# Performance work log

Measured on AMD Instinct MI355X. Metric: run time of the kernel, lower is better.

The kernel has to match this reference:

```python
import jax, jax.numpy as jnp
import numpy as np

B, N, P = 16, 128, 4096          # images, proposals/img, pairs/img
D_IN, D_HID = 1024, 512          # input_dim, hidden_dim
D_GEO, D_EMB = 128, 200          # geometry_feat_dim, embed_dim
N_OBJ, N_REL = 151, 51           # obj classes, rel classes (out_dim = 50)
OUT = N_REL - 1
LN_EPS = 1e-5


def _ln(x, g, b):
    mu = jnp.mean(x, axis=-1, keepdims=True)
    var = jnp.var(x, axis=-1, keepdims=True)
    return (x - mu) * jax.lax.rsqrt(var + LN_EPS) * g + b


def setup_inputs() -> dict:
    key = jax.random.key(0)
    ks = jax.random.split(key, 20)
    w = lambda k, shape: (jax.random.normal(k, shape, jnp.float32) * 0.02)
    return {
        'visual_feat': jax.random.normal(ks[0], (B * P, D_IN), jnp.float32),
        'box_info': jax.random.uniform(ks[1], (B, N, 9), jnp.float32),
        'pred_logits': jax.random.normal(ks[2], (B, N, N_OBJ), jnp.float32),
        'pair_idx': jax.random.randint(ks[3], (B, P, 2), 0, N, jnp.int32),
        'obj_sem_w': w(ks[4], (N_OBJ, D_EMB)),
        'pos_w1': w(ks[5], (9, D_GEO)), 'pos_b1': jnp.zeros((D_GEO,), jnp.float32),
        'pos_w2': w(ks[6], (D_GEO, D_GEO)), 'pos_b2': jnp.zeros((D_GEO,), jnp.float32),
        'vis_w': w(ks[7], (D_IN, D_HID)), 'vis_b': jnp.zeros((D_HID,), jnp.float32),
        'geo_w': w(ks[8], (2 * D_EMB + 2 * D_GEO, D_HID)), 'geo_b': jnp.zeros((D_HID,), jnp.float32),
        'fus_g': jnp.ones((2 * D_HID,), jnp.float32), 'fus_bt': jnp.zeros((2 * D_HID,), jnp.float32),
        'fus_w': w(ks[9], (2 * D_HID, D_HID)), 'fus_b': jnp.zeros((D_HID,), jnp.float32),
        'cls_g': jnp.ones((D_HID,), jnp.float32), 'cls_bt': jnp.zeros((D_HID,), jnp.float32),
        'cls_w': w(ks[10], (D_HID, OUT)), 'cls_b': jnp.zeros((OUT,), jnp.float32),
    }


def reference(visual_feat, box_info, pred_logits, pair_idx,
              obj_sem_w, pos_w1, pos_b1, pos_w2, pos_b2,
              vis_w, vis_b, geo_w, geo_b,
              fus_g, fus_bt, fus_w, fus_b,
              cls_g, cls_bt, cls_w, cls_b):
    # detach() in torch -> stop_gradient
    vf = jax.lax.stop_gradient(visual_feat)
    pl = jax.lax.stop_gradient(pred_logits)
    # vis_embed = Sequential(ReLU, Linear): [B*P, D_IN] -> [B, P, D_HID]
    vis = (jnp.maximum(vf, 0.0) @ vis_w + vis_b).reshape(B, P, D_HID)
    # obj_pos_embed = Linear, ReLU, Linear: [B, N, 9] -> [B, N, D_GEO]
    pos = jnp.maximum(box_info @ pos_w1 + pos_b1, 0.0) @ pos_w2 + pos_b2
    # semantic embed: softmax over obj classes @ embedding table -> [B, N, D_EMB]
    sem = jax.nn.softmax(pl, axis=-1) @ obj_sem_w
    bidx = jnp.arange(B)[:, None]
    s, o = pair_idx[..., 0], pair_idx[..., 1]
    # gather pair reps: [B, P, 2*(D_GEO+D_EMB)]
    rep = jnp.concatenate([pos[bidx, s], sem[bidx, s], pos[bidx, o], sem[bidx, o]], axis=-1)
    # proposal_box_feat_extract = Sequential(ReLU, Linear)
    geo = jnp.maximum(rep, 0.0) @ geo_w + geo_b
    # proposal_feat_fusion = Sequential(LayerNorm, ReLU, Linear)
    fused = jnp.concatenate([vis, geo], axis=-1)
    fused = jnp.maximum(_ln(fused, fus_g, fus_bt), 0.0) @ fus_w + fus_b
    # proposal_relness_cls_fc = Sequential(LayerNorm, ReLU, Linear)
    logits = jnp.maximum(_ln(fused, cls_g, cls_bt), 0.0) @ cls_w + cls_b  # [B, P, OUT]
    # predictor_type == 'single': scatter max sigmoid score into NxN matrix
    scores = jnp.max(jax.nn.sigmoid(logits), axis=-1)  # [B, P]
    rel_mat = jnp.zeros((B, N, N), logits.dtype).at[bidx, s, o].set(scores)
    return logits.reshape(B * P, OUT), rel_mat
```

## Files before the change

### kernel.cpp

```cpp
#include <hip/hip_runtime.h>
#include <cstdint>

#define B_    16
#define N_    128
#define P_    4096
#define M_    65536
#define DIN   1024
#define DHID  512
#define DGEO  128
#define DEMB  200
#define NODEF 328
#define NOBJ  151
#define OUTC  50
#define KGEO  656
#define KGEOP 672

typedef __attribute__((ext_vector_type(8))) short bf16x8;
typedef __attribute__((ext_vector_type(4))) float f32x4;

typedef __attribute__((address_space(3))) unsigned char lds_u8;
typedef __attribute__((address_space(1))) unsigned char glb_u8;

static __device__ __forceinline__ void async_copy16(const void* g, void* l) {
  __builtin_amdgcn_global_load_lds((const glb_u8*)g, (lds_u8*)l, 16, 0, 0);
}

static __device__ __forceinline__ unsigned short f2b(float f) {
  union { float f; unsigned u; } v; v.f = f;
  unsigned r = v.u + 0x7fffu + ((v.u >> 16) & 1u);
  return (unsigned short)(r >> 16);
}
static __device__ __forceinline__ float b2f(unsigned short b) {
  union { unsigned u; float f; } v; v.u = ((unsigned)b) << 16;
  return v.f;
}
static __device__ __forceinline__ unsigned pack2(float a, float b) {
  return (unsigned)f2b(a) | ((unsigned)f2b(b) << 16);
}
static __device__ __forceinline__ void unpack8(uint4 raw, float* x) {
  x[0] = b2f(raw.x & 0xffffu); x[1] = b2f(raw.x >> 16);
  x[2] = b2f(raw.y & 0xffffu); x[3] = b2f(raw.y >> 16);
  x[4] = b2f(raw.z & 0xffffu); x[5] = b2f(raw.z >> 16);
  x[6] = b2f(raw.w & 0xffffu); x[7] = b2f(raw.w >> 16);
}

#define ZN   131072
#define TV   (512 * 1024)
#define TG   (512 * KGEOP)
#define TF   (512 * 1024)
#define TC   (128 * 512)
#define PREP_TOT (ZN + TV + TG + TF + TC)
__global__ __launch_bounds__(256)
void prep_kernel(uint4* __restrict__ scat,
                 const float* __restrict__ vis_w, unsigned short* __restrict__ wT_vis,
                 const float* __restrict__ geo_w, unsigned short* __restrict__ wT_geo,
                 const float* __restrict__ fus_w, unsigned short* __restrict__ wT_fus,
                 const float* __restrict__ cls_w, unsigned short* __restrict__ wT_cls) {
  int idx = blockIdx.x * 256 + threadIdx.x;
  if (idx < ZN) { scat[idx] = make_uint4(0, 0, 0, 0); return; }
  idx -= ZN;
  if (idx < TV) {
    int n = idx >> 10, k = idx & 1023;
    wT_vis[idx] = f2b(vis_w[(size_t)k * 512 + n]);
    return;
  }
  idx -= TV;
  if (idx < TG) {
    int n = idx / KGEOP, k = idx - n * KGEOP;
    wT_geo[idx] = (k < KGEO) ? f2b(geo_w[(size_t)k * 512 + n]) : 0;
    return;
  }
  idx -= TG;
  if (idx < TF) {
    int n = idx >> 10, k = idx & 1023;
    wT_fus[idx] = f2b(fus_w[(size_t)k * 512 + n]);
    return;
  }
  idx -= TF;
  if (idx < TC) {
    int n = idx >> 9, k = idx & 511;
    wT_cls[idx] = (n < OUTC) ? f2b(cls_w[(size_t)k * OUTC + n]) : 0;
  }
}

__global__ __launch_bounds__(128)
void node_kernel(const float* __restrict__ box, const float* __restrict__ plog,
                 const float* __restrict__ semw,
                 const float* __restrict__ w1, const float* __restrict__ b1,
                 const float* __restrict__ w2, const float* __restrict__ b2,
                 unsigned short* __restrict__ nodeFb) {
  const int node = blockIdx.x;
  const int t = threadIdx.x;
  __shared__ float sBox[9];
  __shared__ float sH[128];
  __shared__ float sE[NOBJ];
  __shared__ float sRed[4];
  if (t < 9) sBox[t] = box[node * 9 + t];
  float l0 = (t < NOBJ) ? plog[node * NOBJ + t] : -1e30f;
  float l1 = (t + 128 < NOBJ) ? plog[node * NOBJ + t + 128] : -1e30f;
  __syncthreads();
  float h = b1[t];
#pragma unroll
  for (int i = 0; i < 9; i++) h = fmaf(sBox[i], w1[i * 128 + t], h);
  h = fmaxf(h, 0.f);
  sH[t] = h;
  float mx = fmaxf(l0, l1);
#pragma unroll
  for (int off = 32; off >= 1; off >>= 1) mx = fmaxf(mx, __shfl_xor(mx, off));
  if ((t & 63) == 0) sRed[t >> 6] = mx;
  __syncthreads();
  mx = fmaxf(sRed[0], sRed[1]);
  float e0 = (t < NOBJ) ? expf(l0 - mx) : 0.f;
  float e1 = (t + 128 < NOBJ) ? expf(l1 - mx) : 0.f;
  if (t < NOBJ) sE[t] = e0;
  if (t + 128 < NOBJ) sE[t + 128] = e1;
  float sm = e0 + e1;
#pragma unroll
  for (int off = 32; off >= 1; off >>= 1) sm += __shfl_xor(sm, off);
  if ((t & 63) == 0) sRed[2 + (t >> 6)] = sm;
  __syncthreads();
  const float inv = 1.f / (sRed[2] + sRed[3]);
  float pv = b2[t];
  for (int i = 0; i < 128; i++) pv = fmaf(sH[i], w2[i * 128 + t], pv);
  nodeFb[(size_t)node * NODEF + t] = f2b(fmaxf(pv, 0.f));
  float a0 = 0.f, a1 = 0.f;
  const int d1 = (t + 128 < DEMB) ? (t + 128) : 0;
  for (int i = 0; i < NOBJ; i++) {
    float e = sE[i];
    a0 = fmaf(e, semw[i * DEMB + t], a0);
    a1 = fmaf(e, semw[i * DEMB + d1], a1);
  }
  nodeFb[(size_t)node * NODEF + 128 + t] = f2b(fmaxf(a0 * inv, 0.f));
  if (t + 128 < DEMB) nodeFb[(size_t)node * NODEF + 128 + t + 128] = f2b(fmaxf(a1 * inv, 0.f));
}

__global__ __launch_bounds__(256)
void stats_kernel(const unsigned short* __restrict__ X, float* __restrict__ st) {
  const int lane = threadIdx.x & 63, wv = threadIdx.x >> 6;
  const size_t row = (size_t)blockIdx.x * 4 + wv;
  const unsigned short* xp = X + row * 1024 + lane * 16;
  float x[16];
  uint4 r0 = *(const uint4*)(xp);
  uint4 r1 = *(const uint4*)(xp + 8);
  unpack8(r0, x); unpack8(r1, x + 8);
  float s = 0.f, s2 = 0.f;
#pragma unroll
  for (int q = 0; q < 16; q++) { s += x[q]; s2 = fmaf(x[q], x[q], s2); }
#pragma unroll
  for (int off = 32; off >= 1; off >>= 1) { s += __shfl_xor(s, off); s2 += __shfl_xor(s2, off); }
  if (lane == 0) {
    float mu = s * (1.f / 1024.f);
    float var = s2 * (1.f / 1024.f) - mu * mu;
    ((float2*)st)[row] = make_float2(mu, rsqrtf(var + 1e-5f));
  }
}

template<int D>
__global__ __launch_bounds__(256)
void ln_relu_kernel(unsigned short* __restrict__ X,
                    const float* __restrict__ g, const float* __restrict__ bta) {
  constexpr int C = D / 64;
  const int lane = threadIdx.x & 63, wv = threadIdx.x >> 6;
  const size_t row = (size_t)blockIdx.x * 4 + wv;
  unsigned short* xp = X + row * D + lane * C;
  float x[C];
#pragma unroll
  for (int c = 0; c < C; c += 8) {
    uint4 raw = *(const uint4*)(xp + c);
    unpack8(raw, x + c);
  }
  float s = 0.f, s2 = 0.f;
#pragma unroll
  for (int q = 0; q < C; q++) { s += x[q]; s2 = fmaf(x[q], x[q], s2); }
#pragma unroll
  for (int off = 32; off >= 1; off >>= 1) { s += __shfl_xor(s, off); s2 += __shfl_xor(s2, off); }
  const float mu = s / D;
  const float rs = rsqrtf(s2 / D - mu * mu + 1e-5f);
  const float* gp = g + lane * C;
  const float* bp = bta + lane * C;
#pragma unroll
  for (int c = 0; c < C; c += 8) {
    float4 g0 = *(const float4*)(gp + c), g1 = *(const float4*)(gp + c + 4);
    float4 t0 = *(const float4*)(bp + c), t1 = *(const float4*)(bp + c + 4);
    float y0 = fmaxf(fmaf((x[c + 0] - mu) * rs, g0.x, t0.x), 0.f);
    float y1 = fmaxf(fmaf((x[c + 1] - mu) * rs, g0.y, t0.y), 0.f);
    float y2 = fmaxf(fmaf((x[c + 2] - mu) * rs, g0.z, t0.z), 0.f);
    float y3 = fmaxf(fmaf((x[c + 3] - mu) * rs, g0.w, t0.w), 0.f);
    float y4 = fmaxf(fmaf((x[c + 4] - mu) * rs, g1.x, t1.x), 0.f);
    float y5 = fmaxf(fmaf((x[c + 5] - mu) * rs, g1.y, t1.y), 0.f);
    float y6 = fmaxf(fmaf((x[c + 6] - mu) * rs, g1.z, t1.z), 0.f);
    float y7 = fmaxf(fmaf((x[c + 7] - mu) * rs, g1.w, t1.w), 0.f);
    uint4 u;
    u.x = pack2(y0, y1); u.y = pack2(y2, y3);
    u.z = pack2(y4, y5); u.w = pack2(y6, y7);
    *(uint4*)(xp + c) = u;
  }
}

static __device__ __forceinline__ int pair_swz(int bid, int nwg) {
  const int cpx2 = nwg >> 4;
  const int pr = bid >> 1, q = bid & 1;
  return (((pr & 7) * cpx2) + (pr >> 3)) * 2 + q;
}

template<int MODE>
__global__ __launch_bounds__(512, 4)
void gemm128x256g(const unsigned short* __restrict__ A, int ldaE,
                  const unsigned short* __restrict__ Bt, int Ktot,
                  const float* __restrict__ bias,
                  unsigned short* __restrict__ C, int ldcE, int ccol0,
                  int NS, int NBN,
                  const int* __restrict__ pidx,
                  const unsigned short* __restrict__ nodeFb,
                  const unsigned short* __restrict__ zsrc) {
  __shared__ __align__(16) unsigned char smem[49152];
  const int tid = threadIdx.x;
  const int lane = tid & 63, w = tid >> 6;
  const int swz = pair_swz(blockIdx.x, gridDim.x);
  const int bm = swz / NBN, bn = swz - bm * NBN;

  const int sslot = (tid & 3) ^ ((tid >> 3) & 3);
  const int srow = tid >> 2;
  const size_t ldaBy = (size_t)ldaE * 2, ldbBy = (size_t)Ktot * 2;
  const unsigned char* aG = (const unsigned char*)A + (size_t)(bm * 128 + srow) * ldaBy + sslot * 16;
  const unsigned char* bG = (const unsigned char*)Bt + (size_t)(bn * 256 + srow) * ldbBy + sslot * 16;

  const unsigned short* nbS = nullptr;
  const unsigned short* nbO = nullptr;
  if (MODE == 2) {
    int pr = bm * 128 + srow;
    int2 so = *(const int2*)(pidx + 2 * pr);
    int b = pr >> 12;
    nbS = nodeFb + (size_t)((b << 7) + so.x) * NODEF;
    nbO = nodeFb + (size_t)((b << 7) + so.y) * NODEF;
  }

  auto stage = [&](int s) {
    const int slot = s & 1;
    unsigned char* la = smem + slot * 8192 + w * 1024;
    unsigned char* lb = smem + 16384 + slot * 16384 + w * 1024;
    if (MODE == 0) {
      async_copy16(aG + (size_t)s * 64, la);
    } else {
      const int e = s * 32 + sslot * 8;
      uintptr_t sel = (e < NODEF) ? (uintptr_t)(nbS + e)
                    : (e < KGEO)  ? (uintptr_t)(nbO + (e - NODEF))
                                  : (uintptr_t)zsrc;
      async_copy16((const void*)sel, la);
    }
    const unsigned char* sb = bG + (size_t)s * 64;
    async_copy16(sb, lb);
    async_copy16(sb + 128 * ldbBy, lb + 8192);
  };

  const int wm = w >> 2, wn = w & 3;
  const int frow = lane & 15;
  const int colb = (((lane >> 4) ^ ((frow >> 1) & 3)) << 4);
  const int aRowB = (wm * 64 + frow) * 64;
  const int bRowB = (wn * 64 + frow) * 64;

  f32x4 acc[4][4];
#pragma unroll
  for (int m = 0; m < 4; m++)
#pragma unroll
    for (int n = 0; n < 4; n++) acc[m][n] = (f32x4){0.f, 0.f, 0.f, 0.f};

  stage(0); stage(1);
#pragma unroll 1
  for (int s = 0; s < NS; ++s) {
    if (s == NS - 1) asm volatile("s_waitcnt vmcnt(0)" ::: "memory");
    else             asm volatile("s_waitcnt vmcnt(3)" ::: "memory");
    __builtin_amdgcn_s_barrier();
    __builtin_amdgcn_sched_barrier(0);
    const unsigned char* ab = smem + (s & 1) * 8192;
    const unsigned char* bb = smem + 16384 + (s & 1) * 16384;
    bf16x8 af[4];
#pragma unroll
    for (int m = 0; m < 4; m++) af[m] = *(const bf16x8*)(ab + aRowB + m * 1024 + colb);
    __builtin_amdgcn_s_setprio(1);
#pragma unroll
    for (int n = 0; n < 4; n++) {
      bf16x8 bf = *(const bf16x8*)(bb + bRowB + n * 1024 + colb);
#pragma unroll
      for (int m = 0; m < 4; m++)
        acc[m][n] = __builtin_amdgcn_mfma_f32_16x16x32_bf16(af[m], bf, acc[m][n], 0, 0, 0);
    }
    __builtin_amdgcn_s_setprio(0);
    __builtin_amdgcn_sched_barrier(0);
    __builtin_amdgcn_s_barrier();
    __builtin_amdgcn_sched_barrier(0);
    if (s + 2 < NS) stage(s + 2);
  }
  const int rb = bm * 128 + wm * 64 + ((lane >> 4) << 2);
  const int cb = bn * 256 + wn * 64 + frow;
#pragma unroll
  for (int n = 0; n < 4; n++) {
    const int col = cb + n * 16;
    const float bv = bias[col];
#pragma unroll
    for (int m = 0; m < 4; m++)
#pragma unroll
      for (int i = 0; i < 4; i++) {
        const int row = rb + m * 16 + i;
        C[(size_t)row * ldcE + ccol0 + col] = f2b(acc[m][n][i] + bv);
      }
  }
}

__global__ __launch_bounds__(512, 4)
void gemm256f3(const float* __restrict__ A,
               const unsigned short* __restrict__ Bt,
               const float* __restrict__ bias,
               unsigned short* __restrict__ C, int ldcE, int ccol0,
               int NBN) {
  constexpr int NS = 32;
  __shared__ __align__(16) unsigned char smem[49152];
  const int tid = threadIdx.x;
  const int lane = tid & 63, w = tid >> 6;
  const int swz = pair_swz(blockIdx.x, gridDim.x);
  const int bm = swz / NBN, bn = swz - bm * NBN;

  const int sslot = (tid & 3) ^ ((tid >> 3) & 3);
  const int srow = tid >> 2;
  const float* aG = A + (size_t)(bm * 128 + srow) * 1024 + sslot * 8;
  const unsigned char* bG = (const unsigned char*)Bt + (size_t)(bn * 256 + srow) * 2048 + sslot * 16;
  unsigned char* laBase = smem + srow * 64 + (tid & 3) * 16;
  unsigned char* lbBase = smem + 16384 + w * 1024;

  uint4 ra0[2], ra1[2];

  auto issueA = [&](int s, uint4* ra) {
    const float* p0 = aG + (size_t)s * 32;
    ra[0] = *(const uint4*)(p0);
    ra[1] = *(const uint4*)(p0 + 4);
  };
  auto issueB = [&](int s) {
    const int slot = s & 1;
    const unsigned char* sb = bG + (size_t)s * 64;
    async_copy16(sb, lbBase + slot * 16384);
    async_copy16(sb + 128 * 2048, lbBase + slot * 16384 + 8192);
  };
  auto writeA = [&](int s, const uint4* ra) {
    const int slot = s & 1;
    float x0 = fmaxf(__uint_as_float(ra[0].x), 0.f);
    float x1 = fmaxf(__uint_as_float(ra[0].y), 0.f);
    float x2 = fmaxf(__uint_as_float(ra[0].z), 0.f);
    float x3 = fmaxf(__uint_as_float(ra[0].w), 0.f);
    float x4 = fmaxf(__uint_as_float(ra[1].x), 0.f);
    float x5 = fmaxf(__uint_as_float(ra[1].y), 0.f);
    float x6 = fmaxf(__uint_as_float(ra[1].z), 0.f);
    float x7 = fmaxf(__uint_as_float(ra[1].w), 0.f);
    uint4 u;
    u.x = pack2(x0, x1); u.y = pack2(x2, x3);
    u.z = pack2(x4, x5); u.w = pack2(x6, x7);
    *(uint4*)(laBase + slot * 8192) = u;
  };

  const int wm = w >> 2, wn = w & 3;
  const int frow = lane & 15;
  const int colb = (((lane >> 4) ^ ((frow >> 1) & 3)) << 4);
  const int aRowB = (wm * 64 + frow) * 64;
  const int bRowB = (wn * 64 + frow) * 64;

  f32x4 acc[4][4];
#pragma unroll
  for (int m = 0; m < 4; m++)
#pragma unroll
    for (int n = 0; n < 4; n++) acc[m][n] = (f32x4){0.f, 0.f, 0.f, 0.f};

  issueA(0, ra0); issueB(0);
  issueA(1, ra1); issueB(1);

#pragma unroll 1
  for (int s = 0; s < NS; s += 2) {
#pragma unroll
    for (int half = 0; half < 2; half++) {
      const int sc = s + half;
      uint4* raC = half ? ra1 : ra0;
      if (sc == NS - 1) asm volatile("s_waitcnt vmcnt(0)" ::: "memory");
      else              asm volatile("s_waitcnt vmcnt(4)" ::: "memory");
      __builtin_amdgcn_sched_barrier(0);
      writeA(sc, raC);
      if (sc + 2 < NS) issueA(sc + 2, raC);
      asm volatile("s_waitcnt lgkmcnt(0)" ::: "memory");
      __builtin_amdgcn_s_barrier();
      __builtin_amdgcn_sched_barrier(0);
      const unsigned char* ab = smem + (sc & 1) * 8192;
      const unsigned char* bb = smem + 16384 + (sc & 1) * 16384;
      bf16x8 af[4];
#pragma unroll
      for (int m = 0; m < 4; m++) af[m] = *(const bf16x8*)(ab + aRowB + m * 1024 + colb);
      __builtin_amdgcn_s_setprio(1);
#pragma unroll
      for (int n = 0; n < 4; n++) {
        bf16x8 bf = *(const bf16x8*)(bb + bRowB + n * 1024 + colb);
#pragma unroll
        for (int m = 0; m < 4; m++)
          acc[m][n] = __builtin_amdgcn_mfma_f32_16x16x32_bf16(af[m], bf, acc[m][n], 0, 0, 0);
      }
      __builtin_amdgcn_s_setprio(0);
      __builtin_amdgcn_sched_barrier(0);
      __builtin_amdgcn_s_barrier();
      __builtin_amdgcn_sched_barrier(0);
      if (sc + 2 < NS) issueB(sc + 2);
    }
  }
  const int rb = bm * 128 + wm * 64 + ((lane >> 4) << 2);
  const int cb = bn * 256 + wn * 64 + frow;
#pragma unroll
  for (int n = 0; n < 4; n++) {
    const int col = cb + n * 16;
    const float bv = bias[col];
#pragma unroll
    for (int m = 0; m < 4; m++)
#pragma unroll
      for (int i = 0; i < 4; i++) {
        const int row = rb + m * 16 + i;
        C[(size_t)row * ldcE + ccol0 + col] = f2b(acc[m][n][i] + bv);
      }
  }
}

__global__ __launch_bounds__(512, 4)
void gemm_fusLN(const unsigned short* __restrict__ A,
                const unsigned short* __restrict__ Bt,
                const float* __restrict__ stats,
                const float* __restrict__ lng, const float* __restrict__ lnb,
                const float* __restrict__ bias,
                unsigned short* __restrict__ C,
                int NBN) {
  constexpr int NS = 32;
  __shared__ __align__(16) unsigned char smem[57344];
  const int tid = threadIdx.x;
  const int lane = tid & 63, w = tid >> 6;
  const int swz = pair_swz(blockIdx.x, gridDim.x);
  const int bm = swz / NBN, bn = swz - bm * NBN;

  const int sslot = (tid & 3) ^ ((tid >> 3) & 3);
  const int srow = tid >> 2;
  const unsigned short* aG = A + (size_t)(bm * 128 + srow) * 1024 + sslot * 8;
  const unsigned char* bG = (const unsigned char*)Bt + (size_t)(bn * 256 + srow) * 2048 + sslot * 16;
  unsigned char* laBase = smem + srow * 64 + (tid & 3) * 16;
  unsigned char* lbBase = smem + 16384 + w * 1024;

  {
    const float* src = (w < 4) ? (lng + w * 256 + lane * 4)
                               : (lnb + (w - 4) * 256 + lane * 4);
    unsigned char* dst = smem + 49152 + w * 4096 / 4;
    async_copy16(src, dst);
  }
  asm volatile("s_waitcnt vmcnt(0)" ::: "memory");
  __builtin_amdgcn_s_barrier();

  const float2 st = ((const float2*)stats)[bm * 128 + srow];
  const float mu = st.x, rs = st.y;
  const float* gl = (const float*)(smem + 49152);
  const float* bl = (const float*)(smem + 53248);

  uint4 ra0, ra1;

  auto issueA = [&](int s, uint4* ra) {
    *ra = *(const uint4*)(aG + (size_t)s * 32);
  };
  auto issueB = [&](int s) {
    const int slot = s & 1;
    const unsigned char* sb = bG + (size_t)s * 64;
    async_copy16(sb, lbBase + slot * 16384);
    async_copy16(sb + 128 * 2048, lbBase + slot * 16384 + 8192);
  };
  auto writeA = [&](int s, const uint4* ra) {
    const int slot = s & 1;
    const int k0 = s * 32 + sslot * 8;
    float x[8]; unpack8(*ra, x);
    float4 g0 = *(const float4*)(gl + k0), g1 = *(const float4*)(gl + k0 + 4);
    float4 t0 = *(const float4*)(bl + k0), t1 = *(const float4*)(bl + k0 + 4);
    float y0 = fmaxf(fmaf((x[0] - mu) * rs, g0.x, t0.x), 0.f);
    float y1 = fmaxf(fmaf((x[1] - mu) * rs, g0.y, t0.y), 0.f);
    float y2 = fmaxf(fmaf((x[2] - mu) * rs, g0.z, t0.z), 0.f);
    float y3 = fmaxf(fmaf((x[3] - mu) * rs, g0.w, t0.w), 0.f);
    float y4 = fmaxf(fmaf((x[4] - mu) * rs, g1.x, t1.x), 0.f);
    float y5 = fmaxf(fmaf((x[5] - mu) * rs, g1.y, t1.y), 0.f);
    float y6 = fmaxf(fmaf((x[6] - mu) * rs, g1.z, t1.z), 0.f);
    float y7 = fmaxf(fmaf((x[7] - mu) * rs, g1.w, t1.w), 0.f);
    uint4 u;
    u.x = pack2(y0, y1); u.y = pack2(y2, y3);
    u.z = pack2(y4, y5); u.w = pack2(y6, y7);
    *(uint4*)(laBase + slot * 8192) = u;
  };

  const int wm = w >> 2, wn = w & 3;
  const int frow = lane & 15;
  const int colb = (((lane >> 4) ^ ((frow >> 1) & 3)) << 4);
  const int aRowB = (wm * 64 + frow) * 64;
  const int bRowB = (wn * 64 + frow) * 64;

  f32x4 acc[4][4];
#pragma unroll
  for (int m = 0; m < 4; m++)
#pragma unroll
    for (int n = 0; n < 4; n++) acc[m][n] = (f32x4){0.f, 0.f, 0.f, 0.f};

  issueA(0, &ra0); issueB(0);
  issueA(1, &ra1); issueB(1);

#pragma unroll 1
  for (int s = 0; s < NS; s += 2) {
#pragma unroll
    for (int half = 0; half < 2; half++) {
      const int sc = s + half;
      uint4* raC = half ? &ra1 : &ra0;
      if (sc == NS - 1) asm volatile("s_waitcnt vmcnt(0)" ::: "memory");
      else              asm volatile("s_waitcnt vmcnt(3)" ::: "memory");
      __builtin_amdgcn_sched_barrier(0);
      writeA(sc, raC);
      if (sc + 2 < NS) issueA(sc + 2, raC);
      asm volatile("s_waitcnt lgkmcnt(0)" ::: "memory");
      __builtin_amdgcn_s_barrier();
      __builtin_amdgcn_sched_barrier(0);
      const unsigned char* ab = smem + (sc & 1) * 8192;
      const unsigned char* bb = smem + 16384 + (sc & 1) * 16384;
      bf16x8 af[4];
#pragma unroll
      for (int m = 0; m < 4; m++) af[m] = *(const bf16x8*)(ab + aRowB + m * 1024 + colb);
      __builtin_amdgcn_s_setprio(1);
#pragma unroll
      for (int n = 0; n < 4; n++) {
        bf16x8 bf = *(const bf16x8*)(bb + bRowB + n * 1024 + colb);
#pragma unroll
        for (int m = 0; m < 4; m++)
          acc[m][n] = __builtin_amdgcn_mfma_f32_16x16x32_bf16(af[m], bf, acc[m][n], 0, 0, 0);
      }
      __builtin_amdgcn_s_setprio(0);
      __builtin_amdgcn_sched_barrier(0);
      __builtin_amdgcn_s_barrier();
      __builtin_amdgcn_sched_barrier(0);
      if (sc + 2 < NS) issueB(sc + 2);
    }
  }
  const int rb = bm * 128 + wm * 64 + ((lane >> 4) << 2);
  const int cb = bn * 256 + wn * 64 + frow;
#pragma unroll
  for (int n = 0; n < 4; n++) {
    const int col = cb + n * 16;
    const float bv = bias[col];
#pragma unroll
    for (int m = 0; m < 4; m++)
#pragma unroll
      for (int i = 0; i < 4; i++) {
        const int row = rb + m * 16 + i;
        C[(size_t)row * 512 + col] = f2b(acc[m][n][i] + bv);
      }
  }
}

__global__ __launch_bounds__(256)
void gemm_cls(const unsigned short* __restrict__ A, int lda,
              const unsigned short* __restrict__ Bt,
              const float* __restrict__ bias,
              float* __restrict__ C,
              int Ktot,
              const int* __restrict__ pidx,
              unsigned long long* __restrict__ scat) {
  __shared__ unsigned short ldsA[128 * 64];
  __shared__ unsigned short ldsB[128 * 64];
  const int tid = threadIdx.x;
  const int lane = tid & 63, wid = tid >> 6;
  const int cpx = gridDim.x >> 3;
  const int bm = (blockIdx.x & 7) * cpx + (blockIdx.x >> 3);

  const int srow = wid * 32 + (lane >> 3);
  const int skof = (lane & 7) * 8;
  const unsigned short* ag = A + (size_t)(bm * 128 + srow) * lda + skof;
  const unsigned short* bg = Bt + (size_t)srow * Ktot + skof;

  f32x4 acc[4][4];
#pragma unroll
  for (int m = 0; m < 4; m++)
#pragma unroll
    for (int n = 0; n < 4; n++) acc[m][n] = (f32x4){0.f, 0.f, 0.f, 0.f};

  const int wm = wid >> 1, wn = wid & 1;
  const int frow = lane & 15;
  const int kgrp = (lane >> 4) << 3;

  for (int kt = 0; kt < Ktot; kt += 64) {
#pragma unroll
    for (int i = 0; i < 4; i++) {
      async_copy16(ag + (size_t)i * 8 * lda + kt, &ldsA[wid * 2048 + i * 512]);
      async_copy16(bg + (size_t)i * 8 * Ktot + kt, &ldsB[wid * 2048 + i * 512]);
    }
    __syncthreads();
#pragma unroll
    for (int kk = 0; kk < 64; kk += 32) {
      bf16x8 af[4], bfr[4];
#pragma unroll
      for (int m = 0; m < 4; m++)
        af[m] = *(const bf16x8*)&ldsA[(wm * 64 + m * 16 + frow) * 64 + kk + kgrp];
#pragma unroll
      for (int n = 0; n < 4; n++)
        bfr[n] = *(const bf16x8*)&ldsB[(wn * 64 + n * 16 + frow) * 64 + kk + kgrp];
#pragma unroll
      for (int m = 0; m < 4; m++)
#pragma unroll
        for (int n = 0; n < 4; n++)
          acc[m][n] = __builtin_amdgcn_mfma_f32_16x16x32_bf16(af[m], bfr[n], acc[m][n], 0, 0, 0);
    }
    __syncthreads();
  }
  const int rb = bm * 128 + wm * 64 + ((lane >> 4) << 2);
#pragma unroll
  for (int n = 0; n < 4; n++) {
    const int col = wn * 64 + frow + n * 16;
    const float bv = (col < OUTC) ? bias[col] : 0.f;
#pragma unroll
    for (int m = 0; m < 4; m++)
#pragma unroll
      for (int i = 0; i < 4; i++) {
        const int row = rb + m * 16 + i;
        if (col < OUTC) C[(size_t)row * OUTC + col] = acc[m][n][i] + bv;
      }
  }
  if (wn == 0) {
#pragma unroll
    for (int m = 0; m < 4; m++)
#pragma unroll
      for (int i = 0; i < 4; i++) {
        float mx = -1e30f;
#pragma unroll
        for (int n = 0; n < 4; n++) {
          const int col = n * 16 + frow;
          float v = acc[m][n][i] + ((col < OUTC) ? bias[col] : 0.f);
          if (col < OUTC) mx = fmaxf(mx, v);
        }
        mx = fmaxf(mx, __shfl_xor(mx, 1));
        mx = fmaxf(mx, __shfl_xor(mx, 2));
        mx = fmaxf(mx, __shfl_xor(mx, 4));
        mx = fmaxf(mx, __shfl_xor(mx, 8));
        if (frow == 0) {
          const int row = rb + m * 16 + i;
          float sc = 1.f / (1.f + expf(-mx));
          int b = row >> 12, p = row & 4095;
          int s = pidx[2 * row], o = pidx[2 * row + 1];
          unsigned long long key = (((unsigned long long)(p + 1)) << 32) |
                                   (unsigned long long)__float_as_uint(sc);
          atomicMax(&scat[((size_t)(b * N_ + s) << 7) + o], key);
        }
      }
  }
}

__global__ void relmat_kernel(const unsigned long long* __restrict__ scat, float* __restrict__ out) {
  int i = blockIdx.x * blockDim.x + threadIdx.x;
  if (i >= B_ * N_ * N_) return;
  unsigned long long v = scat[i];
  out[i] = v ? __uint_as_float((unsigned)(v & 0xffffffffu)) : 0.f;
}

extern "C" void kernel_launch(void* const* d_in, const int* in_sizes, int n_in,
                              void* d_out, int out_size, void* d_ws, size_t ws_size,
                              hipStream_t stream) {
  const float* visual_feat = (const float*)d_in[0];
  const float* box_info    = (const float*)d_in[1];
  const float* pred_logits = (const float*)d_in[2];
  const int*   pair_idx    = (const int*)d_in[3];
  const float* obj_sem_w   = (const float*)d_in[4];
  const float* pos_w1 = (const float*)d_in[5];
  const float* pos_b1 = (const float*)d_in[6];
  const float* pos_w2 = (const float*)d_in[7];
  const float* pos_b2 = (const float*)d_in[8];
  const float* vis_w  = (const float*)d_in[9];
  const float* vis_b  = (const float*)d_in[10];
  const float* geo_w  = (const float*)d_in[11];
  const float* geo_b  = (const float*)d_in[12];
  const float* fus_g  = (const float*)d_in[13];
  const float* fus_bt = (const float*)d_in[14];
  const float* fus_w  = (const float*)d_in[15];
  const float* fus_b  = (const float*)d_in[16];
  const float* cls_g  = (const float*)d_in[17];
  const float* cls_bt = (const float*)d_in[18];
  const float* cls_w  = (const float*)d_in[19];
  const float* cls_b  = (const float*)d_in[20];

  char* ws = (char*)d_ws;
  size_t off = 0;
  auto alloc = [&](size_t bytes) { char* p = ws + off; off += (bytes + 255) & ~(size_t)255; return p; };
  unsigned short* fused = (unsigned short*)alloc((size_t)M_ * 1024 * 2);
  unsigned short* fused2 = (unsigned short*)alloc((size_t)M_ * 512 * 2);
  unsigned short* nodeFb = (unsigned short*)alloc((size_t)B_ * N_ * NODEF * 2);
  unsigned short* wT_vis = (unsigned short*)alloc((size_t)512 * 1024 * 2);
  unsigned short* wT_geo = (unsigned short*)alloc((size_t)512 * KGEOP * 2);
  unsigned short* wT_fus = (unsigned short*)alloc((size_t)512 * 1024 * 2);
  unsigned short* wT_cls = (unsigned short*)alloc((size_t)128 * 512 * 2);
  unsigned long long* scat = (unsigned long long*)alloc((size_t)B_ * N_ * N_ * 8);
  float* stats1 = (float*)alloc((size_t)M_ * 2 * 4);

  float* out_logits = (float*)d_out;
  float* out_rel = out_logits + (size_t)M_ * OUTC;

  prep_kernel<<<dim3((PREP_TOT + 255) / 256), 256, 0, stream>>>(
      (uint4*)scat, vis_w, wT_vis, geo_w, wT_geo, fus_w, wT_fus, cls_w, wT_cls);
  node_kernel<<<dim3(B_ * N_), 128, 0, stream>>>(box_info, pred_logits, obj_sem_w,
                                                 pos_w1, pos_b1, pos_w2, pos_b2, nodeFb);
  gemm128x256g<2><<<dim3(1024), 512, 0, stream>>>(nullptr, 0, wT_geo, KGEOP, geo_b,
                                                  fused, 1024, 512, KGEOP / 32, 2,
                                                  pair_idx, nodeFb, (const unsigned short*)scat);
  gemm256f3<<<dim3(1024), 512, 0, stream>>>(visual_feat, wT_vis, vis_b,
                                            fused, 1024, 0, 2);
  stats_kernel<<<dim3(M_ / 4), 256, 0, stream>>>(fused, stats1);
  gemm_fusLN<<<dim3(1024), 512, 0, stream>>>(fused, wT_fus, stats1, fus_g, fus_bt,
                                             fus_b, fused2, 2);
  ln_relu_kernel<512><<<dim3(M_ / 4), 256, 0, stream>>>(fused2, cls_g, cls_bt);
  gemm_cls<<<dim3(512), 256, 0, stream>>>(fused2, 512, wT_cls, cls_b,
                                          out_logits, 512, pair_idx, scat);
  relmat_kernel<<<dim3((B_ * N_ * N_) / 256), 256, 0, stream>>>(scat, out_rel);
}
```

Before: 386.1 us.

## Fuse LayerNorm statistics into GEMM epilogues and LN+ReLU into classifier GEMM

Each GEMM epilogue now emits per-row partial sums and sums of squares into a slotted stats buffer, so the separate stats kernel and the standalone ln_relu pass over fused2 are no longer needed. The consumer GEMMs reduce these partials to get mean and rstd. The classifier GEMM is rewritten to load A through registers and apply LayerNorm+ReLU before writing to LDS, with 512 threads and double buffering. This saves full reads and writes of the activation matrices, at the cost of extra epilogue shuffles, a larger partial-stats buffer, and the loss of the bf16 rounding the old path applied before computing stats.

```diff
diff --git a/kernel.cpp b/kernel.cpp
--- a/kernel.cpp
+++ b/kernel.cpp
@@ -134,85 +134,21 @@
   if (t + 128 < DEMB) nodeFb[(size_t)node * NODEF + 128 + t + 128] = f2b(fmaxf(a1 * inv, 0.f));
 }
 
-__global__ __launch_bounds__(256)
-void stats_kernel(const unsigned short* __restrict__ X, float* __restrict__ st) {
-  const int lane = threadIdx.x & 63, wv = threadIdx.x >> 6;
-  const size_t row = (size_t)blockIdx.x * 4 + wv;
-  const unsigned short* xp = X + row * 1024 + lane * 16;
-  float x[16];
-  uint4 r0 = *(const uint4*)(xp);
-  uint4 r1 = *(const uint4*)(xp + 8);
-  unpack8(r0, x); unpack8(r1, x + 8);
-  float s = 0.f, s2 = 0.f;
-#pragma unroll
-  for (int q = 0; q < 16; q++) { s += x[q]; s2 = fmaf(x[q], x[q], s2); }
-#pragma unroll
-  for (int off = 32; off >= 1; off >>= 1) { s += __shfl_xor(s, off); s2 += __shfl_xor(s2, off); }
-  if (lane == 0) {
-    float mu = s * (1.f / 1024.f);
-    float var = s2 * (1.f / 1024.f) - mu * mu;
-    ((float2*)st)[row] = make_float2(mu, rsqrtf(var + 1e-5f));
-  }
-}
-
-template<int D>
-__global__ __launch_bounds__(256)
-void ln_relu_kernel(unsigned short* __restrict__ X,
-                    const float* __restrict__ g, const float* __restrict__ bta) {
-  constexpr int C = D / 64;
-  const int lane = threadIdx.x & 63, wv = threadIdx.x >> 6;
-  const size_t row = (size_t)blockIdx.x * 4 + wv;
-  unsigned short* xp = X + row * D + lane * C;
-  float x[C];
-#pragma unroll
-  for (int c = 0; c < C; c += 8) {
-    uint4 raw = *(const uint4*)(xp + c);
-    unpack8(raw, x + c);
-  }
-  float s = 0.f, s2 = 0.f;
-#pragma unroll
-  for (int q = 0; q < C; q++) { s += x[q]; s2 = fmaf(x[q], x[q], s2); }
-#pragma unroll
-  for (int off = 32; off >= 1; off >>= 1) { s += __shfl_xor(s, off); s2 += __shfl_xor(s2, off); }
-  const float mu = s / D;
-  const float rs = rsqrtf(s2 / D - mu * mu + 1e-5f);
-  const float* gp = g + lane * C;
-  const float* bp = bta + lane * C;
-#pragma unroll
-  for (int c = 0; c < C; c += 8) {
-    float4 g0 = *(const float4*)(gp + c), g1 = *(const float4*)(gp + c + 4);
-    float4 t0 = *(const float4*)(bp + c), t1 = *(const float4*)(bp + c + 4);
-    float y0 = fmaxf(fmaf((x[c + 0] - mu) * rs, g0.x, t0.x), 0.f);
-    float y1 = fmaxf(fmaf((x[c + 1] - mu) * rs, g0.y, t0.y), 0.f);
-    float y2 = fmaxf(fmaf((x[c + 2] - mu) * rs, g0.z, t0.z), 0.f);
-    float y3 = fmaxf(fmaf((x[c + 3] - mu) * rs, g0.w, t0.w), 0.f);
-    float y4 = fmaxf(fmaf((x[c + 4] - mu) * rs, g1.x, t1.x), 0.f);
-    float y5 = fmaxf(fmaf((x[c + 5] - mu) * rs, g1.y, t1.y), 0.f);
-    float y6 = fmaxf(fmaf((x[c + 6] - mu) * rs, g1.z, t1.z), 0.f);
-    float y7 = fmaxf(fmaf((x[c + 7] - mu) * rs, g1.w, t1.w), 0.f);
-    uint4 u;
-    u.x = pack2(y0, y1); u.y = pack2(y2, y3);
-    u.z = pack2(y4, y5); u.w = pack2(y6, y7);
-    *(uint4*)(xp + c) = u;
-  }
-}
-
 static __device__ __forceinline__ int pair_swz(int bid, int nwg) {
   const int cpx2 = nwg >> 4;
   const int pr = bid >> 1, q = bid & 1;
   return (((pr & 7) * cpx2) + (pr >> 3)) * 2 + q;
 }
 
-template<int MODE>
 __global__ __launch_bounds__(512, 4)
-void gemm128x256g(const unsigned short* __restrict__ A, int ldaE,
-                  const unsigned short* __restrict__ Bt, int Ktot,
-                  const float* __restrict__ bias,
-                  unsigned short* __restrict__ C, int ldcE, int ccol0,
-                  int NS, int NBN,
-                  const int* __restrict__ pidx,
-                  const unsigned short* __restrict__ nodeFb,
-                  const unsigned short* __restrict__ zsrc) {
+void gemm_geo(const unsigned short* __restrict__ Bt, int Ktot,
+              const float* __restrict__ bias,
+              unsigned short* __restrict__ C, int ldcE, int ccol0,
+              int NS, int NBN,
+              const int* __restrict__ pidx,
+              const unsigned short* __restrict__ nodeFb,
+              const unsigned short* __restrict__ zsrc,
+              float2* __restrict__ statsOut) {
   __shared__ __align__(16) unsigned char smem[49152];
   const int tid = threadIdx.x;
   const int lane = tid & 63, w = tid >> 6;
@@ -221,33 +157,24 @@
 
   const int sslot = (tid & 3) ^ ((tid >> 3) & 3);
   const int srow = tid >> 2;
-  const size_t ldaBy = (size_t)ldaE * 2, ldbBy = (size_t)Ktot * 2;
-  const unsigned char* aG = (const unsigned char*)A + (size_t)(bm * 128 + srow) * ldaBy + sslot * 16;
+  const size_t ldbBy = (size_t)Ktot * 2;
   const unsigned char* bG = (const unsigned char*)Bt + (size_t)(bn * 256 + srow) * ldbBy + sslot * 16;
 
-  const unsigned short* nbS = nullptr;
-  const unsigned short* nbO = nullptr;
-  if (MODE == 2) {
-    int pr = bm * 128 + srow;
-    int2 so = *(const int2*)(pidx + 2 * pr);
-    int b = pr >> 12;
-    nbS = nodeFb + (size_t)((b << 7) + so.x) * NODEF;
-    nbO = nodeFb + (size_t)((b << 7) + so.y) * NODEF;
-  }
+  int pr = bm * 128 + srow;
+  int2 so = *(const int2*)(pidx + 2 * pr);
+  int b = pr >> 12;
+  const unsigned short* nbS = nodeFb + (size_t)((b << 7) + so.x) * NODEF;
+  const unsigned short* nbO = nodeFb + (size_t)((b << 7) + so.y) * NODEF;
 
   auto stage = [&](int s) {
     const int slot = s & 1;
     unsigned char* la = smem + slot * 8192 + w * 1024;
     unsigned char* lb = smem + 16384 + slot * 16384 + w * 1024;
-    if (MODE == 0) {
-      async_copy16(aG + (size_t)s * 64, la);
-    } else {
-      const int e = s * 32 + sslot * 8;
-      uintptr_t sel = (e < NODEF) ? (uintptr_t)(nbS + e)
-                    : (e < KGEO)  ? (uintptr_t)(nbO + (e - NODEF))
-                                  : (uintptr_t)zsrc;
-      async_copy16((const void*)sel, la);
-    }
+    const int e = s * 32 + sslot * 8;
+    uintptr_t sel = (e < NODEF) ? (uintptr_t)(nbS + e)
+                  : (e < KGEO)  ? (uintptr_t)(nbO + (e - NODEF))
+                                : (uintptr_t)zsrc;
+    async_copy16((const void*)sel, la);
     const unsigned char* sb = bG + (size_t)s * 64;
     async_copy16(sb, lb);
     async_copy16(sb + 128 * ldbBy, lb + 8192);
@@ -293,18 +220,33 @@
   }
   const int rb = bm * 128 + wm * 64 + ((lane >> 4) << 2);
   const int cb = bn * 256 + wn * 64 + frow;
+  float bv[4];
+#pragma unroll
+  for (int n = 0; n < 4; n++) bv[n] = bias[cb + n * 16];
 #pragma unroll
   for (int n = 0; n < 4; n++) {
     const int col = cb + n * 16;
-    const float bv = bias[col];
 #pragma unroll
     for (int m = 0; m < 4; m++)
 #pragma unroll
-      for (int i = 0; i < 4; i++) {
-        const int row = rb + m * 16 + i;
-        C[(size_t)row * ldcE + ccol0 + col] = f2b(acc[m][n][i] + bv);
+      for (int i = 0; i < 4; i++)
+        C[(size_t)(rb + m * 16 + i) * ldcE + ccol0 + col] = f2b(acc[m][n][i] + bv[n]);
+  }
+  const int slot = 8 + bn * 4 + wn;
+#pragma unroll
+  for (int m = 0; m < 4; m++)
+#pragma unroll
+    for (int i = 0; i < 4; i++) {
+      float s = 0.f, s2 = 0.f;
+#pragma unroll
+      for (int n = 0; n < 4; n++) {
+        float v = acc[m][n][i] + bv[n];
+        s += v; s2 = fmaf(v, v, s2);
       }
-  }
+#pragma unroll
+      for (int off = 1; off <= 8; off <<= 1) { s += __shfl_xor(s, off); s2 += __shfl_xor(s2, off); }
+      if (frow == 0) statsOut[(size_t)(rb + m * 16 + i) * 16 + slot] = make_float2(s, s2);
+    }
 }
 
 __global__ __launch_bounds__(512, 4)
@@ -312,7 +254,7 @@
                const unsigned short* __restrict__ Bt,
                const float* __restrict__ bias,
                unsigned short* __restrict__ C, int ldcE, int ccol0,
-               int NBN) {
+               int NBN, float2* __restrict__ statsOut) {
   constexpr int NS = 32;
   __shared__ __align__(16) unsigned char smem[49152];
   const int tid = threadIdx.x;
@@ -407,28 +349,43 @@
   }
   const int rb = bm * 128 + wm * 64 + ((lane >> 4) << 2);
   const int cb = bn * 256 + wn * 64 + frow;
+  float bv[4];
+#pragma unroll
+  for (int n = 0; n < 4; n++) bv[n] = bias[cb + n * 16];
 #pragma unroll
   for (int n = 0; n < 4; n++) {
     const int col = cb + n * 16;
-    const float bv = bias[col];
 #pragma unroll
     for (int m = 0; m < 4; m++)
 #pragma unroll
-      for (int i = 0; i < 4; i++) {
-        const int row = rb + m * 16 + i;
-        C[(size_t)row * ldcE + ccol0 + col] = f2b(acc[m][n][i] + bv);
+      for (int i = 0; i < 4; i++)
+        C[(size_t)(rb + m * 16 + i) * ldcE + ccol0 + col] = f2b(acc[m][n][i] + bv[n]);
+  }
+  const int slot = bn * 4 + wn;
+#pragma unroll
+  for (int m = 0; m < 4; m++)
+#pragma unroll
+    for (int i = 0; i < 4; i++) {
+      float s = 0.f, s2 = 0.f;
+#pragma unroll
+      for (int n = 0; n < 4; n++) {
+        float v = acc[m][n][i] + bv[n];
+        s += v; s2 = fmaf(v, v, s2);
       }
-  }
+#pragma unroll
+      for (int off = 1; off <= 8; off <<= 1) { s += __shfl_xor(s, off); s2 += __shfl_xor(s2, off); }
+      if (frow == 0) statsOut[(size_t)(rb + m * 16 + i) * 16 + slot] = make_float2(s, s2);
+    }
 }
 
 __global__ __launch_bounds__(512, 4)
 void gemm_fusLN(const unsigned short* __restrict__ A,
                 const unsigned short* __restrict__ Bt,
-                const float* __restrict__ stats,
+                const float2* __restrict__ statsIn,
                 const float* __restrict__ lng, const float* __restrict__ lnb,
                 const float* __restrict__ bias,
                 unsigned short* __restrict__ C,
-                int NBN) {
+                int NBN, float2* __restrict__ statsOut) {
   constexpr int NS = 32;
   __shared__ __align__(16) unsigned char smem[57344];
   const int tid = threadIdx.x;
@@ -446,14 +403,20 @@
   {
     const float* src = (w < 4) ? (lng + w * 256 + lane * 4)
                                : (lnb + (w - 4) * 256 + lane * 4);
-    unsigned char* dst = smem + 49152 + w * 4096 / 4;
+    unsigned char* dst = smem + 49152 + w * 1024;
     async_copy16(src, dst);
   }
   asm volatile("s_waitcnt vmcnt(0)" ::: "memory");
   __builtin_amdgcn_s_barrier();
 
-  const float2 st = ((const float2*)stats)[bm * 128 + srow];
-  const float mu = st.x, rs = st.y;
+  float ssum = 0.f, ssq = 0.f;
+  {
+    const float2* sp = statsIn + (size_t)(bm * 128 + srow) * 16;
+#pragma unroll
+    for (int j = 0; j < 16; j++) { float2 p = sp[j]; ssum += p.x; ssq += p.y; }
+  }
+  const float mu = ssum * (1.f / 1024.f);
+  const float rs = rsqrtf(ssq * (1.f / 1024.f) - mu * mu + 1e-5f);
   const float* gl = (const float*)(smem + 49152);
   const float* bl = (const float*)(smem + 53248);
 
@@ -539,81 +502,160 @@
   }
   const int rb = bm * 128 + wm * 64 + ((lane >> 4) << 2);
   const int cb = bn * 256 + wn * 64 + frow;
+  float bv[4];
+#pragma unroll
+  for (int n = 0; n < 4; n++) bv[n] = bias[cb + n * 16];
 #pragma unroll
   for (int n = 0; n < 4; n++) {
     const int col = cb + n * 16;
-    const float bv = bias[col];
 #pragma unroll
     for (int m = 0; m < 4; m++)
 #pragma unroll
-      for (int i = 0; i < 4; i++) {
-        const int row = rb + m * 16 + i;
-        C[(size_t)row * 512 + col] = f2b(acc[m][n][i] + bv);
+      for (int i = 0; i < 4; i++)
+        C[(size_t)(rb + m * 16 + i) * 512 + col] = f2b(acc[m][n][i] + bv[n]);
+  }
+  const int slot = bn * 4 + wn;
+#pragma unroll
+  for (int m = 0; m < 4; m++)
+#pragma unroll
+    for (int i = 0; i < 4; i++) {
+      float s = 0.f, s2 = 0.f;
+#pragma unroll
+      for (int n = 0; n < 4; n++) {
+        float v = acc[m][n][i] + bv[n];
+        s += v; s2 = fmaf(v, v, s2);
       }
-  }
-}
-
-__global__ __launch_bounds__(256)
-void gemm_cls(const unsigned short* __restrict__ A, int lda,
-              const unsigned short* __restrict__ Bt,
-              const float* __restrict__ bias,
-              float* __restrict__ C,
-              int Ktot,
-              const int* __restrict__ pidx,
-              unsigned long long* __restrict__ scat) {
-  __shared__ unsigned short ldsA[128 * 64];
-  __shared__ unsigned short ldsB[128 * 64];
+#pragma unroll
+      for (int off = 1; off <= 8; off <<= 1) { s += __shfl_xor(s, off); s2 += __shfl_xor(s2, off); }
+      if (frow == 0) statsOut[(size_t)(rb + m * 16 + i) * 8 + slot] = make_float2(s, s2);
+    }
+}
+
+__global__ __launch_bounds__(512, 4)
+void gemm_clsLN(const unsigned short* __restrict__ A,
+                const unsigned short* __restrict__ Bt,
+                const float2* __restrict__ statsIn,
+                const float* __restrict__ lng, const float* __restrict__ lnb,
+                const float* __restrict__ bias,
+                float* __restrict__ C,
+                const int* __restrict__ pidx,
+                unsigned long long* __restrict__ scat) {
+  constexpr int NS = 16;
+  __shared__ __align__(16) unsigned char smem[36864];
   const int tid = threadIdx.x;
-  const int lane = tid & 63, wid = tid >> 6;
+  const int lane = tid & 63, w = tid >> 6;
   const int cpx = gridDim.x >> 3;
   const int bm = (blockIdx.x & 7) * cpx + (blockIdx.x >> 3);
 
-  const int srow = wid * 32 + (lane >> 3);
-  const int skof = (lane & 7) * 8;
-  const unsigned short* ag = A + (size_t)(bm * 128 + srow) * lda + skof;
-  const unsigned short* bg = Bt + (size_t)srow * Ktot + skof;
-
-  f32x4 acc[4][4];
-#pragma unroll
-  for (int m = 0; m < 4; m++)
+  const int sslot = (tid & 3) ^ ((tid >> 3) & 3);
+  const int srow = tid >> 2;
+  const unsigned short* aG = A + (size_t)(bm * 128 + srow) * 512 + sslot * 8;
+  const unsigned char* bG = (const unsigned char*)Bt + (size_t)srow * 1024 + sslot * 16;
+  unsigned char* laBase = smem + srow * 64 + (tid & 3) * 16;
+  unsigned char* lbBase = smem + 16384 + w * 1024;
+
+  if (w < 4) {
+    const float* src = (w < 2) ? (lng + w * 256 + lane * 4)
+                               : (lnb + (w - 2) * 256 + lane * 4);
+    unsigned char* dst = smem + 32768 + ((w < 2) ? w * 1024 : 2048 + (w - 2) * 1024);
+    async_copy16(src, dst);
+  }
+  asm volatile("s_waitcnt vmcnt(0)" ::: "memory");
+  __builtin_amdgcn_s_barrier();
+
+  float ssum = 0.f, ssq = 0.f;
+  {
+    const float2* sp = statsIn + (size_t)(bm * 128 + srow) * 8;
+#pragma unroll
+    for (int j = 0; j < 8; j++) { float2 p = sp[j]; ssum += p.x; ssq += p.y; }
+  }
+  const float mu = ssum * (1.f / 512.f);
+  const float rs = rsqrtf(ssq * (1.f / 512.f) - mu * mu + 1e-5f);
+  const float* gl = (const float*)(smem + 32768);
+  const float* bl = (const float*)(smem + 34816);
+
+  uint4 ra0, ra1;
+  auto issueA = [&](int s, uint4* ra) { *ra = *(const uint4*)(aG + (size_t)s * 32); };
+  auto issueB = [&](int s) {
+    async_copy16(bG + (size_t)s * 64, lbBase + (s & 1) * 8192);
+  };
+  auto writeA = [&](int s, const uint4* ra) {
+    const int slot = s & 1;
+    const int k0 = s * 32 + sslot * 8;
+    float x[8]; unpack8(*ra, x);
+    float4 g0 = *(const float4*)(gl + k0), g1 = *(const float4*)(gl + k0 + 4);
+    float4 t0 = *(const float4*)(bl + k0), t1 = *(const float4*)(bl + k0 + 4);
+    float y0 = fmaxf(fmaf((x[0] - mu) * rs, g0.x, t0.x), 0.f);
+    float y1 = fmaxf(fmaf((x[1] - mu) * rs, g0.y, t0.y), 0.f);
+    float y2 = fmaxf(fmaf((x[2] - mu) * rs, g0.z, t0.z), 0.f);
+    float y3 = fmaxf(fmaf((x[3] - mu) * rs, g0.w, t0.w), 0.f);
+    float y4 = fmaxf(fmaf((x[4] - mu) * rs, g1.x, t1.x), 0.f);
+    float y5 = fmaxf(fmaf((x[5] - mu) * rs, g1.y, t1.y), 0.f);
+    float y6 = fmaxf(fmaf((x[6] - mu) * rs, g1.z, t1.z), 0.f);
+    float y7 = fmaxf(fmaf((x[7] - mu) * rs, g1.w, t1.w), 0.f);
+    uint4 u;
+    u.x = pack2(y0, y1); u.y = pack2(y2, y3);
+    u.z = pack2(y4, y5); u.w = pack2(y6, y7);
+    *(uint4*)(laBase + slot * 8192) = u;
+  };
+
+  const int wm = w >> 1, wn = w & 1;
+  const int frow = lane & 15;
+  const int colb = (((lane >> 4) ^ ((frow >> 1) & 3)) << 4);
+  const int aRowB = (wm * 32 + frow) * 64;
+  const int bRowB = (wn * 64 + frow) * 64;
+
+  f32x4 acc[2][4];
+#pragma unroll
+  for (int m = 0; m < 2; m++)
 #pragma unroll
     for (int n = 0; n < 4; n++) acc[m][n] = (f32x4){0.f, 0.f, 0.f, 0.f};
 
-  const int wm = wid >> 1, wn = wid & 1;
-  const int frow = lane & 15;
-  const int kgrp = (lane >> 4) << 3;
-
-  for (int kt = 0; kt < Ktot; kt += 64) {
-#pragma unroll
-    for (int i = 0; i < 4; i++) {
-      async_copy16(ag + (size_t)i * 8 * lda + kt, &ldsA[wid * 2048 + i * 512]);
-      async_copy16(bg + (size_t)i * 8 * Ktot + kt, &ldsB[wid * 2048 + i * 512]);
+  issueA(0, &ra0); issueB(0);
+  issueA(1, &ra1); issueB(1);
+
+#pragma unroll 1
+  for (int s = 0; s < NS; s += 2) {
+#pragma unroll
+    for (int half = 0; half < 2; half++) {
+      const int sc = s + half;
+      uint4* raC = half ? &ra1 : &ra0;
+      if (sc == NS - 1) asm volatile("s_waitcnt vmcnt(0)" ::: "memory");
+      else              asm volatile("s_waitcnt vmcnt(2)" ::: "memory");
+      __builtin_amdgcn_sched_barrier(0);
+      writeA(sc, raC);
+      if (sc + 2 < NS) issueA(sc + 2, raC);
+      asm volatile("s_waitcnt lgkmcnt(0)" ::: "memory");
+      __builtin_amdgcn_s_barrier();
+      __builtin_amdgcn_sched_barrier(0);
+      const unsigned char* ab = smem + (sc & 1) * 8192;
+      const unsigned char* bb = smem + 16384 + (sc & 1) * 8192;
+      bf16x8 af[2];
+#pragma unroll
+      for (int m = 0; m < 2; m++) af[m] = *(const bf16x8*)(ab + aRowB + m * 1024 + colb);
+      __builtin_amdgcn_s_setprio(1);
+#pragma unroll
+      for (int n = 0; n < 4; n++) {
+        bf16x8 bf = *(const bf16x8*)(bb + bRowB + n * 1024 + colb);
+#pragma unroll
+        for (int m = 0; m < 2; m++)
+          acc[m][n] = __builtin_amdgcn_mfma_f32_16x16x32_bf16(af[m], bf, acc[m][n], 0, 0, 0);
+      }
+      __builtin_amdgcn_s_setprio(0);
+      __builtin_amdgcn_sched_barrier(0);
+      __builtin_amdgcn_s_barrier();
+      __builtin_amdgcn_sched_barrier(0);
+      if (sc + 2 < NS) issueB(sc + 2);
     }
-    __syncthreads();
-#pragma unroll
-    for (int kk = 0; kk < 64; kk += 32) {
-      bf16x8 af[4], bfr[4];
-#pragma unroll
-      for (int m = 0; m < 4; m++)
-        af[m] = *(const bf16x8*)&ldsA[(wm * 64 + m * 16 + frow) * 64 + kk + kgrp];
-#pragma unroll
-      for (int n = 0; n < 4; n++)
-        bfr[n] = *(const bf16x8*)&ldsB[(wn * 64 + n * 16 + frow) * 64 + kk + kgrp];
-#pragma unroll
-      for (int m = 0; m < 4; m++)
-#pragma unroll
-        for (int n = 0; n < 4; n++)
-          acc[m][n] = __builtin_amdgcn_mfma_f32_16x16x32_bf16(af[m], bfr[n], acc[m][n], 0, 0, 0);
-    }
-    __syncthreads();
-  }
-  const int rb = bm * 128 + wm * 64 + ((lane >> 4) << 2);
+  }
+  const int rb = bm * 128 + wm * 32 + ((lane >> 4) << 2);
+  const int cbl = wn * 64 + frow;
 #pragma unroll
   for (int n = 0; n < 4; n++) {
-    const int col = wn * 64 + frow + n * 16;
+    const int col = cbl + n * 16;
     const float bv = (col < OUTC) ? bias[col] : 0.f;
 #pragma unroll
-    for (int m = 0; m < 4; m++)
+    for (int m = 0; m < 2; m++)
 #pragma unroll
       for (int i = 0; i < 4; i++) {
         const int row = rb + m * 16 + i;
@@ -622,7 +664,7 @@
   }
   if (wn == 0) {
 #pragma unroll
-    for (int m = 0; m < 4; m++)
+    for (int m = 0; m < 2; m++)
 #pragma unroll
       for (int i = 0; i < 4; i++) {
         float mx = -1e30f;
@@ -692,7 +734,8 @@
   unsigned short* wT_fus = (unsigned short*)alloc((size_t)512 * 1024 * 2);
   unsigned short* wT_cls = (unsigned short*)alloc((size_t)128 * 512 * 2);
   unsigned long long* scat = (unsigned long long*)alloc((size_t)B_ * N_ * N_ * 8);
-  float* stats1 = (float*)alloc((size_t)M_ * 2 * 4);
+  float2* statsP1 = (float2*)alloc((size_t)M_ * 16 * 8);
+  float2* statsP2 = (float2*)alloc((size_t)M_ * 8 * 8);
 
   float* out_logits = (float*)d_out;
   float* out_rel = out_logits + (size_t)M_ * OUTC;
@@ -701,16 +744,15 @@
       (uint4*)scat, vis_w, wT_vis, geo_w, wT_geo, fus_w, wT_fus, cls_w, wT_cls);
   node_kernel<<<dim3(B_ * N_), 128, 0, stream>>>(box_info, pred_logits, obj_sem_w,
                                                  pos_w1, pos_b1, pos_w2, pos_b2, nodeFb);
-  gemm128x256g<2><<<dim3(1024), 512, 0, stream>>>(nullptr, 0, wT_geo, KGEOP, geo_b,
-                                                  fused, 1024, 512, KGEOP / 32, 2,
-                                                  pair_idx, nodeFb, (const unsigned short*)scat);
+  gemm_geo<<<dim3(1024), 512, 0, stream>>>(wT_geo, KGEOP, geo_b,
+                                           fused, 1024, 512, KGEOP / 32, 2,
+                                           pair_idx, nodeFb, (const unsigned short*)scat,
+                                           statsP1);
   gemm256f3<<<dim3(1024), 512, 0, stream>>>(visual_feat, wT_vis, vis_b,
-                                            fused, 1024, 0, 2);
-  stats_kernel<<<dim3(M_ / 4), 256, 0, stream>>>(fused, stats1);
-  gemm_fusLN<<<dim3(1024), 512, 0, stream>>>(fused, wT_fus, stats1, fus_g, fus_bt,
-                                             fus_b, fused2, 2);
-  ln_relu_kernel<512><<<dim3(M_ / 4), 256, 0, stream>>>(fused2, cls_g, cls_bt);
-  gemm_cls<<<dim3(512), 256, 0, stream>>>(fused2, 512, wT_cls, cls_b,
-                                          out_logits, 512, pair_idx, scat);
+                                            fused, 1024, 0, 2, statsP1);
+  gemm_fusLN<<<dim3(1024), 512, 0, stream>>>(fused, wT_fus, statsP1, fus_g, fus_bt,
+                                             fus_b, fused2, 2, statsP2);
+  gemm_clsLN<<<dim3(512), 512, 0, stream>>>(fused2, wT_cls, statsP2, cls_g, cls_bt,
+                                            cls_b, out_logits, pair_idx, scat);
   relmat_kernel<<<dim3((B_ * N_ * N_) / 256), 256, 0, stream>>>(scat, out_rel);
 }
```

Result: faster. 373.4 us (median of 4 runs) (-3.3%).
